# Kernel optimization log

Measured on AMD Instinct MI355X. Metric: run time of the kernel, lower is better.

## Reference

```python
import jax, jax.numpy as jnp
import numpy as np
from jax import lax

GROUPS = 64

def setup_inputs() -> dict:
    key = jax.random.key(0)
    k1, k2 = jax.random.split(key)
    b, c, d, h, w = 4, 256, 16, 56, 56
    half = c // (2 * GROUPS)  # = 2
    x = jax.random.normal(k1, (b, c, d, h, w), dtype=jnp.float32)
    cweight = jnp.zeros((1, half, d, 1, 1), dtype=jnp.float32)   # init as in torch module
    cbias = jnp.ones((1, half, d, 1, 1), dtype=jnp.float32)
    conv_w = jax.random.normal(k2, (1, 2, 3, 3, 3), dtype=jnp.float32) * 0.05  # OIDHW
    return {"x": x, "cweight": cweight, "cbias": cbias, "conv_w": conv_w}

def reference(x, cweight, cbias, conv_w):
    b, c, d, h, w = x.shape
    xg = x.reshape(b * GROUPS, c // GROUPS, d, h, w)
    half = (c // GROUPS) // 2
    x0, x1 = xg[:, :half], xg[:, half:]
    # channel branch: adaptive avg pool to (d,1,1) == mean over H,W
    xn = jnp.mean(x0, axis=(3, 4), keepdims=True)          # (bg, half, d, 1, 1)
    xn = x0 * jax.nn.sigmoid(cweight * xn + cbias)
    # spatial branch: mean+max over channel, tiny 2->1 conv3d, sigmoid gate
    xs = jnp.concatenate([jnp.mean(x1, axis=1, keepdims=True),
                          jnp.max(x1, axis=1, keepdims=True)], axis=1)  # (bg, 2, d, h, w)
    xs = lax.conv_general_dilated(xs, conv_w, window_strides=(1, 1, 1),
                                  padding='SAME',
                                  dimension_numbers=('NCDHW', 'OIDHW', 'NCDHW'))
    x_out = jax.nn.sigmoid(xs) * x1
    out = jnp.concatenate([xn, x_out], axis=1).reshape(b, c, d, h, w)
    # channel shuffle with groups=2
    out = out.reshape(b, 2, c // 2, d, h, w).transpose(0, 2, 1, 3, 4, 5).reshape(b, c, d, h, w)
    return out
```

## Files before the change

kernel.cpp:

```cpp
#include <hip/hip_runtime.h>
#include <math.h>

#define HW 3136
#define WDIM 56
#define HDIM 56
#define DDIM 16
#define CTOT 256
#define TILE_H 14
#define SROWS 16
#define SW 60

typedef float v4f __attribute__((ext_vector_type(4)));
typedef unsigned int u32;
typedef u32 u32x2 __attribute__((ext_vector_type(2)));
typedef u32 u32x4 __attribute__((ext_vector_type(4)));
typedef __fp16 h2 __attribute__((ext_vector_type(2)));

__device__ __forceinline__ float sigmoidf_(float x) {
    return 1.0f / (1.0f + __expf(-x));
}

__device__ __forceinline__ u32 packh2(float lo, float hi) {
    h2 r = __builtin_amdgcn_cvt_pkrtz(lo, hi);
    union { h2 h; u32 u; } c; c.h = r; return c.u;
}
__device__ __forceinline__ h2 ash2(u32 u) {
    union { u32 u; h2 h; } c; c.u = u; return c.h;
}

__global__ __launch_bounds__(256, 8) void k_all(const float* __restrict__ x,
                                                const float* __restrict__ cw,
                                                const float* __restrict__ cb,
                                                const float* __restrict__ wconv,
                                                float* __restrict__ out) {
    __shared__ __align__(16) u32 ls[4][SROWS][SW];
    __shared__ u32 wsh[27];
    __shared__ float reds[2][4];
    __shared__ float scsh[2];

    const int bid = blockIdx.x;
    const int tid = threadIdx.x;
    const int xcd = bid & 7;
    const int li  = bid >> 3;
    const int gb  = ((li / 48) << 3) + xcd;
    const int r   = li % 48;
    const int bb  = gb >> 6, g = gb & 63;
    const size_t cS = (size_t)DDIM * HW;

    if (r < 16) {
        const int dd = r;

        const float* p0 = x + ((size_t)bb * CTOT + g * 4 + 0) * cS + (size_t)dd * HW;
        const float* p1 = x + ((size_t)bb * CTOT + g * 4 + 1) * cS + (size_t)dd * HW;

        v4f a0 = __builtin_nontemporal_load((const v4f*)(p0 + 4 * (tid)));
        v4f a1 = __builtin_nontemporal_load((const v4f*)(p0 + 4 * (tid + 256)));
        v4f a2 = __builtin_nontemporal_load((const v4f*)(p0 + 4 * (tid + 512)));
        v4f b0 = __builtin_nontemporal_load((const v4f*)(p1 + 4 * (tid)));
        v4f b1 = __builtin_nontemporal_load((const v4f*)(p1 + 4 * (tid + 256)));
        v4f b2 = __builtin_nontemporal_load((const v4f*)(p1 + 4 * (tid + 512)));
        v4f a3 = (v4f){0.f, 0.f, 0.f, 0.f}, b3 = a3;
        if (tid < 16) {
            a3 = __builtin_nontemporal_load((const v4f*)(p0 + 4 * (tid + 768)));
            b3 = __builtin_nontemporal_load((const v4f*)(p1 + 4 * (tid + 768)));
        }

        float s0 = (a0[0]+a0[1]+a0[2]+a0[3]) + (a1[0]+a1[1]+a1[2]+a1[3])
                 + (a2[0]+a2[1]+a2[2]+a2[3]) + (a3[0]+a3[1]+a3[2]+a3[3]);
        float s1 = (b0[0]+b0[1]+b0[2]+b0[3]) + (b1[0]+b1[1]+b1[2]+b1[3])
                 + (b2[0]+b2[1]+b2[2]+b2[3]) + (b3[0]+b3[1]+b3[2]+b3[3]);
        #pragma unroll
        for (int off = 32; off > 0; off >>= 1) {
            s0 += __shfl_down(s0, off, 64);
            s1 += __shfl_down(s1, off, 64);
        }
        const int lane = tid & 63, wave = tid >> 6;
        if (lane == 0) { reds[0][wave] = s0; reds[1][wave] = s1; }
        __syncthreads();
        if (tid == 0) {
            const float m0 = (reds[0][0]+reds[0][1]+reds[0][2]+reds[0][3]) * (1.0f / HW);
            const float m1 = (reds[1][0]+reds[1][1]+reds[1][2]+reds[1][3]) * (1.0f / HW);
            scsh[0] = sigmoidf_(cw[0 * DDIM + dd] * m0 + cb[0 * DDIM + dd]);
            scsh[1] = sigmoidf_(cw[1 * DDIM + dd] * m1 + cb[1 * DDIM + dd]);
        }
        __syncthreads();
        const float sc0 = scsh[0], sc1 = scsh[1];

        const int cs0 = g * 4 + 0, cs1 = g * 4 + 1;
        const int co0 = 2 * (cs0 & 127) + (cs0 >> 7);
        const int co1 = 2 * (cs1 & 127) + (cs1 >> 7);
        float* o0 = out + ((size_t)bb * CTOT + co0) * cS + (size_t)dd * HW;
        float* o1 = out + ((size_t)bb * CTOT + co1) * cS + (size_t)dd * HW;

        #pragma unroll
        for (int p = 0; p < 4; ++p) { a0[p] *= sc0; a1[p] *= sc0; a2[p] *= sc0; a3[p] *= sc0;
                                      b0[p] *= sc1; b1[p] *= sc1; b2[p] *= sc1; b3[p] *= sc1; }
        __builtin_nontemporal_store(a0, (v4f*)(o0 + 4 * (tid)));
        __builtin_nontemporal_store(a1, (v4f*)(o0 + 4 * (tid + 256)));
        __builtin_nontemporal_store(a2, (v4f*)(o0 + 4 * (tid + 512)));
        __builtin_nontemporal_store(b0, (v4f*)(o1 + 4 * (tid)));
        __builtin_nontemporal_store(b1, (v4f*)(o1 + 4 * (tid + 256)));
        __builtin_nontemporal_store(b2, (v4f*)(o1 + 4 * (tid + 512)));
        if (tid < 16) {
            __builtin_nontemporal_store(a3, (v4f*)(o0 + 4 * (tid + 768)));
            __builtin_nontemporal_store(b3, (v4f*)(o1 + 4 * (tid + 768)));
        }
        return;
    }

    const int j   = r - 16;
    const int th  = j & 3;
    const int ddp = j >> 2;
    const int dd0 = 2 * ddp;
    const int r0  = th * TILE_H;

    if (tid < 27) wsh[tid] = packh2(wconv[tid], wconv[27 + tid]);
    if (tid < 128) {
        const int wp = tid >> 5, rr = (tid >> 1) & 15;
        ls[wp][rr][(tid & 1) ? 57 : 0] = 0u;
    }

    const float* xb = x + ((size_t)bb * CTOT + g * 4) * cS;
    const float* pa = xb + 2 * cS;
    const float* pb = xb + 3 * cS;

    for (int it = tid; it < 4 * SROWS * 14; it += 256) {
        const int row = it / 14, qd = it - row * 14;
        const int wp = row >> 4, rr = row & 15;
        const int dz = dd0 + wp - 1;
        const int gr = r0 + rr - 1;
        const int gc0 = 4 * qd;
        u32 m0, m1, m2, m3;
        if (((unsigned)dz < DDIM) & ((unsigned)gr < HDIM)) {
            const size_t o = (size_t)dz * HW + gr * WDIM + gc0;
            const v4f a = *(const v4f*)(pa + o);
            const v4f b = *(const v4f*)(pb + o);
            m0 = packh2(0.5f * (a[0] + b[0]), fmaxf(a[0], b[0]));
            m1 = packh2(0.5f * (a[1] + b[1]), fmaxf(a[1], b[1]));
            m2 = packh2(0.5f * (a[2] + b[2]), fmaxf(a[2], b[2]));
            m3 = packh2(0.5f * (a[3] + b[3]), fmaxf(a[3], b[3]));
        } else {
            m0 = m1 = m2 = m3 = 0u;
        }
        u32* wr = &ls[wp][rr][1 + gc0];
        wr[0] = m0; wr[1] = m1; wr[2] = m2; wr[3] = m3;
    }
    __syncthreads();

    if (tid < TILE_H * 14) {
        const int hh = tid / 14;
        const int ww = 4 * (tid - hh * 14);

        float acc0[4] = {0.f, 0.f, 0.f, 0.f};
        float acc1[4] = {0.f, 0.f, 0.f, 0.f};

        #pragma unroll
        for (int wp = 0; wp < 4; ++wp) {
            #pragma unroll
            for (int kh = 0; kh < 3; ++kh) {
                const u32* rp = &ls[wp][hh + kh][ww];
                const u32x4 q  = *(const u32x4*)rp;
                const u32x2 q2 = *(const u32x2*)(rp + 4);
                const u32 vv[6] = {q[0], q[1], q[2], q[3], q2[0], q2[1]};
                if (wp < 3) {
                    #pragma unroll
                    for (int kw = 0; kw < 3; ++kw) {
                        const h2 wv = ash2(wsh[wp * 9 + kh * 3 + kw]);
                        #pragma unroll
                        for (int p = 0; p < 4; ++p)
                            acc0[p] = __builtin_amdgcn_fdot2(ash2(vv[p + kw]), wv, acc0[p], false);
                    }
                }
                if (wp >= 1) {
                    #pragma unroll
                    for (int kw = 0; kw < 3; ++kw) {
                        const h2 wv = ash2(wsh[(wp - 1) * 9 + kh * 3 + kw]);
                        #pragma unroll
                        for (int p = 0; p < 4; ++p)
                            acc1[p] = __builtin_amdgcn_fdot2(ash2(vv[p + kw]), wv, acc1[p], false);
                    }
                }
            }
        }

        const int cs2 = g * 4 + 2, cs3 = g * 4 + 3;
        const int co2 = 2 * (cs2 & 127) + (cs2 >> 7);
        const int co3 = 2 * (cs3 & 127) + (cs3 >> 7);

        const int s = (r0 + hh) * WDIM + ww;
        float* outb = out + (size_t)bb * CTOT * cS + s;
        #pragma unroll
        for (int pl = 0; pl < 2; ++pl) {
            const float* acc = pl ? acc1 : acc0;
            const size_t po = (size_t)(dd0 + pl) * HW;
            const v4f v1a = *(const v4f*)(pa + po + s);
            const v4f v1b = *(const v4f*)(pb + po + s);
            v4f o2, o3;
            #pragma unroll
            for (int p = 0; p < 4; ++p) {
                const float sig = sigmoidf_(acc[p]);
                o2[p] = v1a[p] * sig;
                o3[p] = v1b[p] * sig;
            }
            __builtin_nontemporal_store(o2, (v4f*)(outb + (size_t)co2 * cS + po));
            __builtin_nontemporal_store(o3, (v4f*)(outb + (size_t)co3 * cS + po));
        }
    }
}

extern "C" void kernel_launch(void* const* d_in, const int* in_sizes, int n_in,
                              void* d_out, int out_size, void* d_ws, size_t ws_size,
                              hipStream_t stream) {
    const float* x     = (const float*)d_in[0];
    const float* cw    = (const float*)d_in[1];
    const float* cb    = (const float*)d_in[2];
    const float* wconv = (const float*)d_in[3];
    float* out = (float*)d_out;

    k_all<<<dim3(12288), 256, 0, stream>>>(x, cw, cb, wconv, out);
}
```

Measured before the change: 71.64 us.

## Compute four depth planes per spatial block to cut halo reloads

Each spatial-branch block now produces four output depth planes from six staged input planes instead of two from four, which shrinks the grid from 12288 to 8192 blocks. This lowers the redundant halo reads of neighbouring depth planes and the per-block setup cost. The channel branch also drops its second barrier, so every thread computes the sigmoid scale directly from the shared partial sums. In exchange, LDS use per block rises, the launch-bounds occupancy hint drops from 8 to 7, and each thread holds more accumulator registers.

```diff
diff --git a/kernel.cpp b/kernel.cpp
--- a/kernel.cpp
+++ b/kernel.cpp
@@ -9,6 +9,7 @@
 #define TILE_H 14
 #define SROWS 16
 #define SW 60
+#define WPL 6
 
 typedef float v4f __attribute__((ext_vector_type(4)));
 typedef unsigned int u32;
@@ -28,22 +29,21 @@
     union { u32 u; h2 h; } c; c.u = u; return c.h;
 }
 
-__global__ __launch_bounds__(256, 8) void k_all(const float* __restrict__ x,
+__global__ __launch_bounds__(256, 7) void k_all(const float* __restrict__ x,
                                                 const float* __restrict__ cw,
                                                 const float* __restrict__ cb,
                                                 const float* __restrict__ wconv,
                                                 float* __restrict__ out) {
-    __shared__ __align__(16) u32 ls[4][SROWS][SW];
+    __shared__ __align__(16) u32 ls[WPL][SROWS][SW];
     __shared__ u32 wsh[27];
     __shared__ float reds[2][4];
-    __shared__ float scsh[2];
 
     const int bid = blockIdx.x;
     const int tid = threadIdx.x;
     const int xcd = bid & 7;
     const int li  = bid >> 3;
-    const int gb  = ((li / 48) << 3) + xcd;
-    const int r   = li % 48;
+    const int gb  = ((li >> 5) << 3) + xcd;
+    const int r   = li & 31;
     const int bb  = gb >> 6, g = gb & 63;
     const size_t cS = (size_t)DDIM * HW;
 
@@ -77,14 +77,10 @@
         const int lane = tid & 63, wave = tid >> 6;
         if (lane == 0) { reds[0][wave] = s0; reds[1][wave] = s1; }
         __syncthreads();
-        if (tid == 0) {
-            const float m0 = (reds[0][0]+reds[0][1]+reds[0][2]+reds[0][3]) * (1.0f / HW);
-            const float m1 = (reds[1][0]+reds[1][1]+reds[1][2]+reds[1][3]) * (1.0f / HW);
-            scsh[0] = sigmoidf_(cw[0 * DDIM + dd] * m0 + cb[0 * DDIM + dd]);
-            scsh[1] = sigmoidf_(cw[1 * DDIM + dd] * m1 + cb[1 * DDIM + dd]);
-        }
-        __syncthreads();
-        const float sc0 = scsh[0], sc1 = scsh[1];
+        const float m0 = (reds[0][0]+reds[0][1]+reds[0][2]+reds[0][3]) * (1.0f / HW);
+        const float m1 = (reds[1][0]+reds[1][1]+reds[1][2]+reds[1][3]) * (1.0f / HW);
+        const float sc0 = sigmoidf_(cw[0 * DDIM + dd] * m0 + cb[0 * DDIM + dd]);
+        const float sc1 = sigmoidf_(cw[1 * DDIM + dd] * m1 + cb[1 * DDIM + dd]);
 
         const int cs0 = g * 4 + 0, cs1 = g * 4 + 1;
         const int co0 = 2 * (cs0 & 127) + (cs0 >> 7);
@@ -110,13 +106,13 @@
 
     const int j   = r - 16;
     const int th  = j & 3;
-    const int ddp = j >> 2;
-    const int dd0 = 2 * ddp;
+    const int dq  = j >> 2;
+    const int dd0 = 4 * dq;
     const int r0  = th * TILE_H;
 
     if (tid < 27) wsh[tid] = packh2(wconv[tid], wconv[27 + tid]);
-    if (tid < 128) {
-        const int wp = tid >> 5, rr = (tid >> 1) & 15;
+    if (tid < 192) {
+        const int wp = tid / 32, rr = (tid >> 1) & 15;
         ls[wp][rr][(tid & 1) ? 57 : 0] = 0u;
     }
 
@@ -124,7 +120,7 @@
     const float* pa = xb + 2 * cS;
     const float* pb = xb + 3 * cS;
 
-    for (int it = tid; it < 4 * SROWS * 14; it += 256) {
+    for (int it = tid; it < WPL * SROWS * 14; it += 256) {
         const int row = it / 14, qd = it - row * 14;
         const int wp = row >> 4, rr = row & 15;
         const int dz = dd0 + wp - 1;
@@ -151,33 +147,28 @@
         const int hh = tid / 14;
         const int ww = 4 * (tid - hh * 14);
 
-        float acc0[4] = {0.f, 0.f, 0.f, 0.f};
-        float acc1[4] = {0.f, 0.f, 0.f, 0.f};
-
-        #pragma unroll
-        for (int wp = 0; wp < 4; ++wp) {
+        float acc[4][4] = {{0.f,0.f,0.f,0.f},{0.f,0.f,0.f,0.f},
+                           {0.f,0.f,0.f,0.f},{0.f,0.f,0.f,0.f}};
+
+        #pragma unroll
+        for (int wp = 0; wp < WPL; ++wp) {
             #pragma unroll
             for (int kh = 0; kh < 3; ++kh) {
                 const u32* rp = &ls[wp][hh + kh][ww];
                 const u32x4 q  = *(const u32x4*)rp;
                 const u32x2 q2 = *(const u32x2*)(rp + 4);
                 const u32 vv[6] = {q[0], q[1], q[2], q[3], q2[0], q2[1]};
-                if (wp < 3) {
-                    #pragma unroll
-                    for (int kw = 0; kw < 3; ++kw) {
-                        const h2 wv = ash2(wsh[wp * 9 + kh * 3 + kw]);
+                #pragma unroll
+                for (int op = 0; op < 4; ++op) {
+                    const int kd = wp - op;
+                    if (kd >= 0 && kd < 3) {
                         #pragma unroll
-                        for (int p = 0; p < 4; ++p)
-                            acc0[p] = __builtin_amdgcn_fdot2(ash2(vv[p + kw]), wv, acc0[p], false);
-                    }
-                }
-                if (wp >= 1) {
-                    #pragma unroll
-                    for (int kw = 0; kw < 3; ++kw) {
-                        const h2 wv = ash2(wsh[(wp - 1) * 9 + kh * 3 + kw]);
-                        #pragma unroll
-                        for (int p = 0; p < 4; ++p)
-                            acc1[p] = __builtin_amdgcn_fdot2(ash2(vv[p + kw]), wv, acc1[p], false);
+                        for (int kw = 0; kw < 3; ++kw) {
+                            const h2 wv = ash2(wsh[kd * 9 + kh * 3 + kw]);
+                            #pragma unroll
+                            for (int p = 0; p < 4; ++p)
+                                acc[op][p] = __builtin_amdgcn_fdot2(ash2(vv[p + kw]), wv, acc[op][p], false);
+                        }
                     }
                 }
             }
@@ -190,15 +181,14 @@
         const int s = (r0 + hh) * WDIM + ww;
         float* outb = out + (size_t)bb * CTOT * cS + s;
         #pragma unroll
-        for (int pl = 0; pl < 2; ++pl) {
-            const float* acc = pl ? acc1 : acc0;
-            const size_t po = (size_t)(dd0 + pl) * HW;
+        for (int op = 0; op < 4; ++op) {
+            const size_t po = (size_t)(dd0 + op) * HW;
             const v4f v1a = *(const v4f*)(pa + po + s);
             const v4f v1b = *(const v4f*)(pb + po + s);
             v4f o2, o3;
             #pragma unroll
             for (int p = 0; p < 4; ++p) {
-                const float sig = sigmoidf_(acc[p]);
+                const float sig = sigmoidf_(acc[op][p]);
                 o2[p] = v1a[p] * sig;
                 o3[p] = v1b[p] * sig;
             }
@@ -217,5 +207,5 @@
     const float* wconv = (const float*)d_in[3];
     float* out = (float*)d_out;
 
-    k_all<<<dim3(12288), 256, 0, stream>>>(x, cw, cb, wconv, out);
-}
+    k_all<<<dim3(8192), 256, 0, stream>>>(x, cw, cb, wconv, out);
+}
```

Measured after the change: 72.25 us. No clear change (+0.9%).
